# Kernel tuning notes

Hardware: AMD Instinct MI355X
Metric: run time of the kernel (lower is better)

## Reference

```python
import jax, jax.numpy as jnp
import numpy as np


def polymatmul(x, d):
    """Matrix multiply of 2x2 matrices whose entries are polynomials.

    x: (b, n, 2, 2, d1)  -- batch of per-diagonal-block 2x2 polynomial matrices
    d: (n, 2, 2, d2)     -- per-block 2x2 polynomial matrices (the diagonal params)
    Returns: (b, n, 2, 2, d1 + d2 - 1)
    out[b,n,i,j,:] = sum_k full_conv(x[b,n,i,k,:], d[n,k,j,:])
    Implemented by looping over the (small) d2 coefficient axis and accumulating
    shifted 2x2 matmuls, so the only large intermediate is the output itself.
    """
    d1 = x.shape[-1]
    d2 = d.shape[-1]
    out = jnp.zeros(x.shape[:-1] + (d1 + d2 - 1,), dtype=x.dtype)
    for v in range(d2):
        # contract over k (the inner 2-dim), broadcast over poly coeff axis u
        term = jnp.einsum('bniku,nkj->bniju', x, d[..., v])
        out = out.at[..., v:v + d1].add(term)
    return out


def setup_inputs() -> dict:
    key = jax.random.key(0)
    k1, k2, k3 = jax.random.split(key, 3)
    size, deg = 8192, 7
    b, d1 = 64, 16
    input_ = jax.random.normal(k1, (b, 2 * size, 2, 2, d1), dtype=jnp.float32)
    diag1 = jax.random.normal(k2, (size, 2, 2, deg + 1), dtype=jnp.float32)
    diag2 = jax.random.normal(k3, (size, 2, 2, deg + 1), dtype=jnp.float32)
    return {"input_": input_, "diag1": diag1, "diag2": diag2}


def reference(input_, diag1, diag2):
    size = diag1.shape[0]
    # HstackDiag.forward: sum of the two polynomial block-diagonal matmuls
    return polymatmul(input_[:, :size], diag1) + polymatmul(input_[:, size:], diag2)
```

## Files before the change

### kernel.cpp

```cpp
#include <hip/hip_runtime.h>

#define BB 64
#define NN 8192
#define TILE 64
#define DOUT 23

__global__ __launch_bounds__(256) void hstackdiag_kernel(
    const float* __restrict__ input,
    const float* __restrict__ diag1,
    const float* __restrict__ diag2,
    float* __restrict__ out) {
    __shared__ float4 sbuf[2048];

    const int t = threadIdx.x;
    const int bx = blockIdx.x;
    const int b = bx >> 7;
    const int n0 = (bx & 127) * TILE;

    const float4* g1 = (const float4*)input + ((size_t)b * (2 * NN) + n0) * 16;
    const float4* g2 = g1 + (size_t)NN * 16;

    float4 r1[4], r2[4];
#pragma unroll
    for (int r = 0; r < 4; ++r) r1[r] = g1[r * 256 + t];
#pragma unroll
    for (int r = 0; r < 4; ++r) r2[r] = g2[r * 256 + t];
#pragma unroll
    for (int r = 0; r < 4; ++r) {
        const int G = r * 256 + t;
        const int L = G ^ ((G >> 3) & 7);
        sbuf[L] = r1[r];
    }
#pragma unroll
    for (int r = 0; r < 4; ++r) {
        const int G = r * 256 + t;
        const int L = G ^ ((G >> 3) & 7);
        sbuf[1024 + L] = r2[r];
    }
    __syncthreads();

    const int j = t & 1;
    const int i = (t >> 1) & 1;
    const int unit = t >> 2;
    const int n = n0 + unit;

    const float4* dp1 = (const float4*)diag1 + (size_t)n * 8 + j * 2;
    const float4* dp2 = (const float4*)diag2 + (size_t)n * 8 + j * 2;

    float acc[DOUT];
#pragma unroll
    for (int u = 0; u < DOUT; ++u) acc[u] = 0.0f;

#pragma unroll
    for (int h = 0; h < 2; ++h) {
        const int sb = h * 1024;
        const float4* dp = (h == 0) ? dp1 : dp2;
#pragma unroll
        for (int k = 0; k < 2; ++k) {
            float4 dq0 = dp[k * 4 + 0];
            float4 dq1 = dp[k * 4 + 1];
            float dv[8] = {dq0.x, dq0.y, dq0.z, dq0.w,
                           dq1.x, dq1.y, dq1.z, dq1.w};

            float xv[16];
#pragma unroll
            for (int q = 0; q < 4; ++q) {
                const int Gc = unit * 16 + i * 8 + k * 4 + q;
                const int Lc = Gc ^ ((Gc >> 3) & 7);
                float4 xq = sbuf[sb + Lc];
                xv[q * 4 + 0] = xq.x;
                xv[q * 4 + 1] = xq.y;
                xv[q * 4 + 2] = xq.z;
                xv[q * 4 + 3] = xq.w;
            }
#pragma unroll
            for (int v = 0; v < 8; ++v) {
                const float c = dv[v];
#pragma unroll
                for (int u = 0; u < 16; ++u) {
                    acc[u + v] += xv[u] * c;
                }
            }
        }
    }

    __syncthreads();
    float* sout = (float*)sbuf;
#pragma unroll
    for (int q = 0; q < DOUT; ++q) {
        sout[t * DOUT + q] = acc[q];
    }
    __syncthreads();
    float* gout = out + ((size_t)b * NN + n0) * (4 * DOUT);
#pragma unroll
    for (int r = 0; r < DOUT; ++r) {
        gout[r * 256 + t] = sout[r * 256 + t];
    }
}

extern "C" void kernel_launch(void* const* d_in, const int* in_sizes, int n_in,
                              void* d_out, int out_size, void* d_ws, size_t ws_size,
                              hipStream_t stream) {
    const float* input = (const float*)d_in[0];
    const float* diag1 = (const float*)d_in[1];
    const float* diag2 = (const float*)d_in[2];
    float* out = (float*)d_out;

    const int grid = BB * (NN / TILE);
    hstackdiag_kernel<<<grid, 256, 0, stream>>>(input, diag1, diag2, out);
}
```

Before: 88.48 us.

## Halve shared memory by staging input halves sequentially and chunking output writeback

The kernel now stages the two input halves one at a time through a 16KB shared buffer instead of a 32KB buffer, and writes the output back in two 32-unit chunks so it fits the smaller buffer. The goal is more resident blocks per CU and fewer registers live at once, which should help hide memory latency. In exchange it adds extra barriers and serialises the second half's global load behind the first half's compute, which removes overlap within a block.

```diff
diff --git a/kernel.cpp b/kernel.cpp
--- a/kernel.cpp
+++ b/kernel.cpp
@@ -5,12 +5,37 @@
 #define TILE 64
 #define DOUT 23
 
+__device__ __forceinline__ void compute_half(const float4* __restrict__ sbuf,
+                                             const float4* __restrict__ dp,
+                                             int unit, int i, float acc[DOUT]) {
+#pragma unroll
+    for (int k = 0; k < 2; ++k) {
+        float4 dq0 = dp[k * 4 + 0];
+        float4 dq1 = dp[k * 4 + 1];
+        const float dv[8] = {dq0.x, dq0.y, dq0.z, dq0.w,
+                             dq1.x, dq1.y, dq1.z, dq1.w};
+#pragma unroll
+        for (int q = 0; q < 4; ++q) {
+            const int G = unit * 16 + i * 8 + k * 4 + q;
+            float4 xq = sbuf[G ^ ((G >> 3) & 7)];
+            const float xe[4] = {xq.x, xq.y, xq.z, xq.w};
+#pragma unroll
+            for (int e = 0; e < 4; ++e) {
+#pragma unroll
+                for (int v = 0; v < 8; ++v) {
+                    acc[q * 4 + e + v] += xe[e] * dv[v];
+                }
+            }
+        }
+    }
+}
+
 __global__ __launch_bounds__(256) void hstackdiag_kernel(
     const float* __restrict__ input,
     const float* __restrict__ diag1,
     const float* __restrict__ diag2,
     float* __restrict__ out) {
-    __shared__ float4 sbuf[2048];
+    __shared__ float4 sbuf[1024];
 
     const int t = threadIdx.x;
     const int bx = blockIdx.x;
@@ -20,30 +45,10 @@
     const float4* g1 = (const float4*)input + ((size_t)b * (2 * NN) + n0) * 16;
     const float4* g2 = g1 + (size_t)NN * 16;
 
-    float4 r1[4], r2[4];
-#pragma unroll
-    for (int r = 0; r < 4; ++r) r1[r] = g1[r * 256 + t];
-#pragma unroll
-    for (int r = 0; r < 4; ++r) r2[r] = g2[r * 256 + t];
-#pragma unroll
-    for (int r = 0; r < 4; ++r) {
-        const int G = r * 256 + t;
-        const int L = G ^ ((G >> 3) & 7);
-        sbuf[L] = r1[r];
-    }
-#pragma unroll
-    for (int r = 0; r < 4; ++r) {
-        const int G = r * 256 + t;
-        const int L = G ^ ((G >> 3) & 7);
-        sbuf[1024 + L] = r2[r];
-    }
-    __syncthreads();
-
     const int j = t & 1;
     const int i = (t >> 1) & 1;
     const int unit = t >> 2;
     const int n = n0 + unit;
-
     const float4* dp1 = (const float4*)diag1 + (size_t)n * 8 + j * 2;
     const float4* dp2 = (const float4*)diag2 + (size_t)n * 8 + j * 2;
 
@@ -51,50 +56,55 @@
 #pragma unroll
     for (int u = 0; u < DOUT; ++u) acc[u] = 0.0f;
 
+    {
+        float4 r[4];
 #pragma unroll
-    for (int h = 0; h < 2; ++h) {
-        const int sb = h * 1024;
-        const float4* dp = (h == 0) ? dp1 : dp2;
+        for (int rr = 0; rr < 4; ++rr) r[rr] = g1[rr * 256 + t];
 #pragma unroll
-        for (int k = 0; k < 2; ++k) {
-            float4 dq0 = dp[k * 4 + 0];
-            float4 dq1 = dp[k * 4 + 1];
-            float dv[8] = {dq0.x, dq0.y, dq0.z, dq0.w,
-                           dq1.x, dq1.y, dq1.z, dq1.w};
-
-            float xv[16];
-#pragma unroll
-            for (int q = 0; q < 4; ++q) {
-                const int Gc = unit * 16 + i * 8 + k * 4 + q;
-                const int Lc = Gc ^ ((Gc >> 3) & 7);
-                float4 xq = sbuf[sb + Lc];
-                xv[q * 4 + 0] = xq.x;
-                xv[q * 4 + 1] = xq.y;
-                xv[q * 4 + 2] = xq.z;
-                xv[q * 4 + 3] = xq.w;
-            }
-#pragma unroll
-            for (int v = 0; v < 8; ++v) {
-                const float c = dv[v];
-#pragma unroll
-                for (int u = 0; u < 16; ++u) {
-                    acc[u + v] += xv[u] * c;
-                }
-            }
+        for (int rr = 0; rr < 4; ++rr) {
+            const int G = rr * 256 + t;
+            sbuf[G ^ ((G >> 3) & 7)] = r[rr];
         }
     }
+    __syncthreads();
+
+    compute_half(sbuf, dp1, unit, i, acc);
 
     __syncthreads();
-    float* sout = (float*)sbuf;
+
+    {
+        float4 r[4];
 #pragma unroll
-    for (int q = 0; q < DOUT; ++q) {
-        sout[t * DOUT + q] = acc[q];
+        for (int rr = 0; rr < 4; ++rr) r[rr] = g2[rr * 256 + t];
+#pragma unroll
+        for (int rr = 0; rr < 4; ++rr) {
+            const int G = rr * 256 + t;
+            sbuf[G ^ ((G >> 3) & 7)] = r[rr];
+        }
     }
     __syncthreads();
+
+    compute_half(sbuf, dp2, unit, i, acc);
+
+    __syncthreads();
+
+    float* sout = (float*)sbuf;
+    const int c = i * 2 + j;
     float* gout = out + ((size_t)b * NN + n0) * (4 * DOUT);
+
 #pragma unroll
-    for (int r = 0; r < DOUT; ++r) {
-        gout[r * 256 + t] = sout[r * 256 + t];
+    for (int p = 0; p < 2; ++p) {
+        if ((unit >> 5) == p) {
+#pragma unroll
+            for (int q = 0; q < DOUT; ++q)
+                sout[(unit & 31) * 92 + c * DOUT + q] = acc[q];
+        }
+        __syncthreads();
+#pragma unroll
+        for (int rr = 0; rr < 11; ++rr)
+            gout[p * 2944 + rr * 256 + t] = sout[rr * 256 + t];
+        if (t < 128) gout[p * 2944 + 2816 + t] = sout[2816 + t];
+        if (p == 0) __syncthreads();
     }
 }
 
```

Result: no change. 88.08 us (-0.5%).
